# Kernel optimization log

Measured on AMD Instinct MI355X. Metric: run time of the kernel, lower is better.

## Reference

```python
import jax, jax.numpy as jnp
import numpy as np

ALPHA = 40.0
BETA = 2.0
MARGIN = 0.5
N = 8192
D = 128
NUM_CLASSES = 64


def setup_inputs() -> dict:
    key = jax.random.key(0)
    k1, k2 = jax.random.split(key)
    x = jax.random.normal(k1, (N, D), dtype=jnp.float32)
    # L2-normalize embeddings (standard for this metric-learning loss; keeps
    # sim in [-1,1] so sim[i,i]==1 is excluded by the `< 1` filter and the
    # exponentials stay finite, as in real training).
    x = x / jnp.linalg.norm(x, axis=1, keepdims=True)
    targets = jax.random.randint(k2, (N,), 0, NUM_CLASSES, dtype=jnp.int64)
    return {"inputs": x, "targets": targets}


def reference(inputs, targets):
    # sim[i,j] = <x_i, x_j>  -- [n, n]
    sim = jnp.matmul(inputs, inputs.T)
    same = targets[:, None] == targets[None, :]          # same-class mask
    pos_mask = same & (sim < 1.0)                        # positives (drops self pair)
    neg_mask = ~same                                     # negatives

    BIG = jnp.float32(1e30)
    # hardest (smallest) positive and hardest (largest) negative per row
    min_pos = jnp.min(jnp.where(pos_mask, sim, BIG), axis=1)   # [n]
    max_neg = jnp.max(jnp.where(neg_mask, sim, -BIG), axis=1)  # [n]

    # hard mining: keep negatives close to the hardest positive and
    # positives close to the hardest negative (0.1 slack), matching the
    # per-row sort/threshold logic of the original loop.
    neg_keep = neg_mask & (sim + 0.1 > min_pos[:, None])
    pos_keep = pos_mask & (sim - 0.1 < max_neg[:, None])

    p_cnt = jnp.sum(pos_keep, axis=1)                    # [n]
    n_cnt = jnp.sum(neg_keep, axis=1)                    # [n]
    valid = (p_cnt >= 1) & (n_cnt >= 1)                  # rows not skipped

    zp = -BETA * (sim - MARGIN)
    zn = ALPHA * (sim - MARGIN)
    pos_loss = (2.0 / BETA) * jnp.log1p(jnp.exp(zp))     # 2/beta*log(1+e^{-beta(s-m)})
    neg_loss = (2.0 / ALPHA) * jnp.log1p(jnp.exp(zn))    # 2/alpha*log(1+e^{alpha(s-m)})

    # d mean(pos_loss)/d s = -(2/P) * sigmoid(-beta(s-m)); analog for negatives
    p_div = jnp.maximum(p_cnt, 1).astype(sim.dtype)[:, None]
    n_div = jnp.maximum(n_cnt, 1).astype(sim.dtype)[:, None]
    pos_grad = -(2.0 / p_div) * jax.nn.sigmoid(zp)
    neg_grad = (2.0 / n_div) * jax.nn.sigmoid(zn)

    wp = pos_keep & valid[:, None]
    wn = neg_keep & valid[:, None]
    zero = jnp.zeros((), sim.dtype)
    pair_loss = jnp.where(wp, pos_loss, zero) + jnp.where(wn, neg_loss, zero)
    pair_grad = jnp.where(wp, pos_grad, zero) + jnp.where(wn, neg_grad, zero)
    return pair_loss.reshape(-1), pair_grad.reshape(-1)
```

## Files before the change

kernel.cpp:

```cpp
#include <hip/hip_runtime.h>
#include <hip/hip_fp16.h>

#define NN 8192
#define DD 128

typedef _Float16 f16x8 __attribute__((ext_vector_type(8)));
typedef float f32x4 __attribute__((ext_vector_type(4)));

__global__ __launch_bounds__(256) void prep_kernel(const float* __restrict__ X,
                                                   _Float16* __restrict__ Xc) {
  const int t = blockIdx.x * 256 + threadIdx.x;
  const size_t base = (size_t)t * 8;
  const int row = (int)(base >> 7);
  const int col = (int)(base & 127);
  float4 a = *(const float4*)&X[base];
  float4 b = *(const float4*)&X[base + 4];
  const float av[8] = {a.x, a.y, a.z, a.w, b.x, b.y, b.z, b.w};
  f16x8 h, l;
#pragma unroll
  for (int e = 0; e < 8; ++e) {
    const _Float16 hh = (_Float16)av[e];
    h[e] = hh;
    l[e] = (_Float16)(av[e] - (float)hh);
  }
  *(f16x8*)&Xc[(size_t)row * 256 + col] = h;
  *(f16x8*)&Xc[(size_t)row * 256 + 128 + col] = l;
}

__global__ __launch_bounds__(256, 4) void sim_mfma_kernel(
    const _Float16* __restrict__ Xc, float* __restrict__ simOut) {
  __shared__ char smem[32768];

  const int flat = blockIdx.x;
  const int swz = (flat & 7) * 512 + (flat >> 3);
  const int i0 = (swz >> 6) << 7;
  const int j0 = (swz & 63) << 7;

  const int tid = threadIdx.x;
  const int lane = tid & 63;
  const int w = tid >> 6;
  const int m = lane & 15, kq = lane >> 4;
  const int wr = w >> 1, wc = w & 1;

  int sg_off[4];
  int sd_off[4];
  int sg_row[4];
#pragma unroll
  for (int it = 0; it < 4; ++it) {
    const int C = it * 256 + tid;
    const int tile = C >> 9;
    const int cc = C & 511;
    const int r = cc >> 2;
    const int k4 = cc & 3;
    const int k4p = k4 ^ (r & 3);
    sg_row[it] = (tile ? j0 : i0) + r;
    sg_off[it] = k4p << 4;
    sd_off[it] = tile * 8192 + cc * 16;
  }

#define STAGE(ks, b)                                                         \
  {                                                                          \
    _Pragma("unroll") for (int it = 0; it < 4; ++it) {                       \
      const char* g = (const char*)Xc + ((size_t)sg_row[it] << 9) +          \
                      (ks)*64 + sg_off[it];                                  \
      __builtin_amdgcn_global_load_lds(                                      \
          (const __attribute__((address_space(1))) void*)g,                  \
          (__attribute__((address_space(3))) void*)(smem + (b)*16384 +       \
                                                    sd_off[it]),             \
          16, 0, 0);                                                         \
    }                                                                        \
  }

  f32x4 acc[4][4] = {};

  STAGE(0, 0);
  __syncthreads();

#pragma unroll
  for (int ks = 0; ks < 8; ++ks) {
    const int b = ks & 1;
    if (ks < 7) STAGE(ks + 1, b ^ 1);
    const _Float16* As = (const _Float16*)(smem + b * 16384);
    const _Float16* Bs = (const _Float16*)(smem + b * 16384 + 8192);
    f16x8 af[4], bf[4];
#pragma unroll
    for (int f = 0; f < 4; ++f) {
      const int R = wr * 64 + f * 16 + m;
      af[f] = *(const f16x8*)(As + R * 32 + ((kq ^ (R & 3)) << 3));
    }
#pragma unroll
    for (int g = 0; g < 4; ++g) {
      const int R = wc * 64 + g * 16 + m;
      bf[g] = *(const f16x8*)(Bs + R * 32 + ((kq ^ (R & 3)) << 3));
    }
#pragma unroll
    for (int f = 0; f < 4; ++f)
#pragma unroll
      for (int g = 0; g < 4; ++g)
        acc[f][g] = __builtin_amdgcn_mfma_f32_16x16x32_f16(af[f], bf[g],
                                                           acc[f][g], 0, 0, 0);
    __syncthreads();
  }
#undef STAGE

  float* Tr = (float*)smem;
#pragma unroll
  for (int ph = 0; ph < 2; ++ph) {
    if (ph) __syncthreads();
    if (wr == ph) {
#pragma unroll
      for (int f = 0; f < 4; ++f)
#pragma unroll
        for (int g = 0; g < 4; ++g)
#pragma unroll
          for (int rg = 0; rg < 4; ++rg)
            Tr[(f * 16 + kq * 4 + rg) * 128 + wc * 64 + g * 16 + m] =
                acc[f][g][rg];
    }
    __syncthreads();
#pragma unroll
    for (int it = 0; it < 8; ++it) {
      const int F = it * 256 + tid;
      const int row = F >> 5;
      const int c4 = (F & 31) * 4;
      const float4 v = *(const float4*)&Tr[row * 128 + c4];
      *(float4*)&simOut[(size_t)(i0 + ph * 64 + row) * NN + j0 + c4] = v;
    }
  }
}

__global__ __launch_bounds__(256) void row_kernel(const float* simG,
                                                  const int* __restrict__ tgt,
                                                  float* lossG,
                                                  float* gradG) {
  __shared__ unsigned char tg[NN];
  __shared__ float redA[4];
  __shared__ float redB[4];
  const int i = blockIdx.x;
  const int tid = threadIdx.x;
  const size_t rowOff = (size_t)i * NN;

  for (int b = tid * 4; b < NN; b += 1024) {
    int4 t4 = *(const int4*)&tgt[b];
    tg[b + 0] = (unsigned char)t4.x;
    tg[b + 1] = (unsigned char)t4.y;
    tg[b + 2] = (unsigned char)t4.z;
    tg[b + 3] = (unsigned char)t4.w;
  }
  const unsigned char tci = (unsigned char)tgt[i];

  float4 sv[8];
#pragma unroll
  for (int q = 0; q < 8; ++q)
    sv[q] = *(const float4*)&simG[rowOff + (size_t)(tid * 4 + q * 1024)];
  __syncthreads();

  unsigned mmask = 0;
  float lmin = 1e30f, lmax = -1e30f;
#pragma unroll
  for (int q = 0; q < 8; ++q) {
    uchar4 t4 = *(const uchar4*)&tg[tid * 4 + q * 1024];
    const unsigned char tt[4] = {t4.x, t4.y, t4.z, t4.w};
    const float* sp = (const float*)&sv[q];
#pragma unroll
    for (int e = 0; e < 4; ++e) {
      const bool same = (tt[e] == tci);
      const float s = sp[e];
      if (same) {
        mmask |= (1u << (q * 4 + e));
        if (s < 1.0f) lmin = fminf(lmin, s);
      } else {
        lmax = fmaxf(lmax, s);
      }
    }
  }
#pragma unroll
  for (int off = 32; off > 0; off >>= 1) {
    lmin = fminf(lmin, __shfl_down(lmin, off));
    lmax = fmaxf(lmax, __shfl_down(lmax, off));
  }
  if ((tid & 63) == 0) {
    redA[tid >> 6] = lmin;
    redB[tid >> 6] = lmax;
  }
  __syncthreads();
  const float minpos = fminf(fminf(redA[0], redA[1]), fminf(redA[2], redA[3]));
  const float maxneg = fmaxf(fmaxf(redB[0], redB[1]), fmaxf(redB[2], redB[3]));
  __syncthreads();

  float pc = 0.f, nc = 0.f;
#pragma unroll
  for (int q = 0; q < 8; ++q) {
    const float* sp = (const float*)&sv[q];
#pragma unroll
    for (int e = 0; e < 4; ++e) {
      const bool same = (mmask >> (q * 4 + e)) & 1u;
      const float s = sp[e];
      if (same) {
        if (s < 1.0f && (s - 0.1f) < maxneg) pc += 1.f;
      } else {
        if ((s + 0.1f) > minpos) nc += 1.f;
      }
    }
  }
#pragma unroll
  for (int off = 32; off > 0; off >>= 1) {
    pc += __shfl_down(pc, off);
    nc += __shfl_down(nc, off);
  }
  if ((tid & 63) == 0) {
    redA[tid >> 6] = pc;
    redB[tid >> 6] = nc;
  }
  __syncthreads();
  const float pcnt = redA[0] + redA[1] + redA[2] + redA[3];
  const float ncnt = redB[0] + redB[1] + redB[2] + redB[3];
  const bool valid = (pcnt >= 1.f) && (ncnt >= 1.f);
  const float cp = -2.f / fmaxf(pcnt, 1.f);
  const float cn = 2.f / fmaxf(ncnt, 1.f);

#pragma unroll
  for (int q = 0; q < 8; ++q) {
    const float* sp = (const float*)&sv[q];
    float lo[4], go[4];
#pragma unroll
    for (int e = 0; e < 4; ++e) {
      const float s = sp[e];
      const bool same = (mmask >> (q * 4 + e)) & 1u;
      bool keep = same ? (s < 1.0f && (s - 0.1f) < maxneg)
                       : ((s + 0.1f) > minpos);
      keep = keep && valid;
      const float z = same ? fmaf(-2.f, s, 1.f) : fmaf(40.f, s, -20.f);
      const float ez = __expf(z);
      const float d = 1.f + ez;
      const float ll = __logf(d);
      const float sig = __fdividef(ez, d);
      const float lv = same ? ll : 0.05f * ll;
      const float gv = (same ? cp : cn) * sig;
      lo[e] = keep ? lv : 0.f;
      go[e] = keep ? gv : 0.f;
    }
    const size_t a = rowOff + (size_t)(tid * 4 + q * 1024);
    f32x4 lv4 = {lo[0], lo[1], lo[2], lo[3]};
    f32x4 gv4 = {go[0], go[1], go[2], go[3]};
    __builtin_nontemporal_store(lv4, (f32x4*)&lossG[a]);
    __builtin_nontemporal_store(gv4, (f32x4*)&gradG[a]);
  }
}

extern "C" void kernel_launch(void* const* d_in, const int* in_sizes, int n_in,
                              void* d_out, int out_size, void* d_ws,
                              size_t ws_size, hipStream_t stream) {
  const float* X = (const float*)d_in[0];
  const int* tgt = (const int*)d_in[1];
  float* out = (float*)d_out;
  float* lossG = out;
  float* gradG = out + (size_t)NN * NN;

  _Float16* Xc = (_Float16*)lossG;

  hipLaunchKernelGGL(prep_kernel, dim3(NN * DD / (256 * 8)), dim3(256), 0,
                     stream, X, Xc);
  hipLaunchKernelGGL(sim_mfma_kernel, dim3(64 * 64), dim3(256), 0, stream, Xc,
                     gradG);
  hipLaunchKernelGGL(row_kernel, dim3(NN), dim3(256), 0, stream, gradG, tgt,
                     lossG, gradG);
}
```

Measured before the change: 209.3 us.

## Exploit similarity symmetry by computing only upper-triangle tiles and mirroring

The similarity kernel now skips tiles below the diagonal. Each off-diagonal block computes its tile once and writes it twice: directly, and transposed through shared memory into the mirrored position. This halves the MFMA and operand-load work of the GEMM stage. The shared-memory staging buffer is padded to a row stride of 133 floats so the transposed writes avoid bank conflicts. The downside is that float4 LDS reads become misaligned, and the transposed epilogue adds extra synchronisation to a stage that is dominated by stores.

```diff
diff --git a/kernel.cpp b/kernel.cpp
--- a/kernel.cpp
+++ b/kernel.cpp
@@ -29,12 +29,14 @@
 
 __global__ __launch_bounds__(256, 4) void sim_mfma_kernel(
     const _Float16* __restrict__ Xc, float* __restrict__ simOut) {
-  __shared__ char smem[32768];
+  __shared__ char smem[64 * 133 * 4];
 
   const int flat = blockIdx.x;
   const int swz = (flat & 7) * 512 + (flat >> 3);
-  const int i0 = (swz >> 6) << 7;
-  const int j0 = (swz & 63) << 7;
+  const int ti = swz >> 6, tj = swz & 63;
+  if (tj < ti) return;
+  const int i0 = ti << 7;
+  const int j0 = tj << 7;
 
   const int tid = threadIdx.x;
   const int lane = tid & 63;
@@ -42,9 +44,7 @@
   const int m = lane & 15, kq = lane >> 4;
   const int wr = w >> 1, wc = w & 1;
 
-  int sg_off[4];
-  int sd_off[4];
-  int sg_row[4];
+  int sg_off[4], sd_off[4], sg_row[4];
 #pragma unroll
   for (int it = 0; it < 4; ++it) {
     const int C = it * 256 + tid;
@@ -104,6 +104,7 @@
 #undef STAGE
 
   float* Tr = (float*)smem;
+
 #pragma unroll
   for (int ph = 0; ph < 2; ++ph) {
     if (ph) __syncthreads();
@@ -114,7 +115,7 @@
         for (int g = 0; g < 4; ++g)
 #pragma unroll
           for (int rg = 0; rg < 4; ++rg)
-            Tr[(f * 16 + kq * 4 + rg) * 128 + wc * 64 + g * 16 + m] =
+            Tr[(f * 16 + kq * 4 + rg) * 133 + wc * 64 + g * 16 + m] =
                 acc[f][g][rg];
     }
     __syncthreads();
@@ -123,8 +124,34 @@
       const int F = it * 256 + tid;
       const int row = F >> 5;
       const int c4 = (F & 31) * 4;
-      const float4 v = *(const float4*)&Tr[row * 128 + c4];
+      const float4 v = *(const float4*)&Tr[row * 133 + c4];
       *(float4*)&simOut[(size_t)(i0 + ph * 64 + row) * NN + j0 + c4] = v;
+    }
+  }
+
+  if (i0 == j0) return;
+
+#pragma unroll
+  for (int mph = 0; mph < 2; ++mph) {
+    __syncthreads();
+    if (wc == mph) {
+#pragma unroll
+      for (int f = 0; f < 4; ++f)
+#pragma unroll
+        for (int g = 0; g < 4; ++g)
+#pragma unroll
+          for (int rg = 0; rg < 4; ++rg)
+            Tr[(g * 16 + m) * 133 + wr * 64 + f * 16 + kq * 4 + rg] =
+                acc[f][g][rg];
+    }
+    __syncthreads();
+#pragma unroll
+    for (int it = 0; it < 8; ++it) {
+      const int F = it * 256 + tid;
+      const int row = F >> 5;
+      const int c4 = (F & 31) * 4;
+      const float4 v = *(const float4*)&Tr[row * 133 + c4];
+      *(float4*)&simOut[(size_t)(j0 + mph * 64 + row) * NN + i0 + c4] = v;
     }
   }
 }
```

New measurement: 223.5 us. 1.07x slower.
